# Performance work log

Measured on AMD Instinct MI355X. Metric: run time of the kernel, lower is better.

## Reference

```python
import jax, jax.numpy as jnp
import numpy as np

K = 3; STRIDE = 1; PAD = 1; DIL = 1; DG = 1


def _conv(x, w, b):
    y = jax.lax.conv_general_dilated(
        x, w, (STRIDE, STRIDE), [(PAD, PAD), (PAD, PAD)],
        dimension_numbers=("NCHW", "OIHW", "NCHW"))
    return y + b[None, :, None, None]


def _dcnv2(x, offset, mask, w, b):
    # x: [B,C,H,W]; offset: [B,2*DG*K*K,Ho,Wo]; mask: [B,DG*K*K,Ho,Wo] (post-sigmoid)
    B, C, H, W = x.shape
    Ho, Wo = offset.shape[2], offset.shape[3]
    KK = K * K
    Cdg = C // DG
    off = offset.reshape(B, DG, KK, 2, Ho, Wo)
    off_y, off_x = off[:, :, :, 0], off[:, :, :, 1]          # [B,DG,KK,Ho,Wo]
    m = mask.reshape(B, DG, KK, Ho, Wo)
    ky = (jnp.arange(KK) // K) * DIL
    kx = (jnp.arange(KK) % K) * DIL
    base_y = jnp.arange(Ho) * STRIDE - PAD
    base_x = jnp.arange(Wo) * STRIDE - PAD
    py = (base_y[None, :, None] + ky[:, None, None]).astype(x.dtype)  # [KK,Ho,1]
    px = (base_x[None, None, :] + kx[:, None, None]).astype(x.dtype)  # [KK,1,Wo]
    sy = py[None, None] + off_y                               # [B,DG,KK,Ho,Wo]
    sx = px[None, None] + off_x
    y0 = jnp.floor(sy); x0 = jnp.floor(sx)
    wy = sy - y0; wx = sx - x0
    feat = x.reshape(B, DG, Cdg, H * W)

    def corner(iy, ix):
        valid = (iy >= 0) & (iy <= H - 1) & (ix >= 0) & (ix <= W - 1)
        iyc = jnp.clip(iy, 0, H - 1).astype(jnp.int32)
        ixc = jnp.clip(ix, 0, W - 1).astype(jnp.int32)
        idx = (iyc * W + ixc).reshape(B, DG, KK * Ho * Wo)
        g = jax.vmap(jax.vmap(lambda f, i: f[:, i]))(feat, idx)  # [B,DG,Cdg,KK*Ho*Wo]
        g = g.reshape(B, DG, Cdg, KK, Ho, Wo)
        return g * valid[:, :, None].astype(x.dtype)

    one = jnp.asarray(1.0, x.dtype)
    v = (corner(y0, x0) * ((one - wy) * (one - wx))[:, :, None]
         + corner(y0, x0 + 1) * ((one - wy) * wx)[:, :, None]
         + corner(y0 + 1, x0) * (wy * (one - wx))[:, :, None]
         + corner(y0 + 1, x0 + 1) * (wy * wx)[:, :, None])
    v = v * m[:, :, None]                                     # modulation
    wg = w.reshape(w.shape[0], DG, Cdg, KK)                    # [Cout,DG,Cdg,KK]
    out = jnp.einsum("bgckhw,ogck->bohw", v, wg) + b[None, :, None, None]
    return out


def setup_inputs() -> dict:
    key = jax.random.key(0)
    k1, k2, k3 = jax.random.split(key, 3)
    B, C, H, W, Cout = 8, 256, 64, 64, 256
    x = jax.random.normal(k1, (B, C, H, W), jnp.float32)
    w_off = jax.random.normal(k2, (DG * 3 * K * K, C, K, K), jnp.float32) * 0.01
    b_off = jnp.zeros((DG * 3 * K * K,), jnp.float32)
    w_dcn = jax.random.normal(k3, (Cout, C, K, K), jnp.float32) * 0.02
    b_dcn = jnp.zeros((Cout,), jnp.float32)
    return {"x": x, "w_off": w_off, "b_off": b_off, "w_dcn": w_dcn, "b_dcn": b_dcn}


def reference(x, w_off, b_off, w_dcn, b_dcn):
    om = _conv(x, w_off, b_off)                # [B,3*DG*K*K,Ho,Wo]
    o1, o2, mask = jnp.split(om, 3, axis=1)
    offset = jnp.concatenate([o1, o2], axis=1)
    mask = jax.nn.sigmoid(mask)
    return _dcnv2(x, offset, mask, w_dcn, b_dcn)
```

## Files before the change

### kernel.cpp

```cpp
#include <hip/hip_runtime.h>
#include <math.h>

#define BB 8
#define CIN 256
#define HW 4096
#define BHW 32768
#define COUT 256
#define KTOT 2304
#define WS_N (BB*9*HW)

#define WOFF2_OFF (4*WS_N)
#define ACC_OFF   (WOFF2_OFF + 64512)
#define ATOMIC_NEED ((size_t)(ACC_OFF + 27*BHW) * 4)
#define XT_OFF    (ACC_OFF + 27*BHW)
#define NEED3     ((size_t)(XT_OFF + (BB*HW*CIN)/2) * 4)
#define WO16_OFF  (XT_OFF + (BB*HW*CIN)/2)
#define NEED4     ((size_t)(WO16_OFF + 36864) * 4)

#define PQ 520
#define NK2 36

typedef _Float16 hf;
typedef __attribute__((ext_vector_type(8))) _Float16 hfx8;
typedef __attribute__((ext_vector_type(4))) float f32x4;

__global__ __launch_bounds__(256) void prep_kernel(
    const float* __restrict__ x, const float* __restrict__ w_dcn,
    const float* __restrict__ w_off,
    hf* __restrict__ xt, hf* __restrict__ w16, hf* __restrict__ wo16)
{
  __shared__ float t[64][65];
  const int bx = blockIdx.x;
  const int tid = threadIdx.x;

  if (bx < 2048) {
    const int b  = bx >> 8;
    const int cb = (bx & 255) >> 6;
    const int pb = bx & 63;
    const int hi = tid >> 6, lo = tid & 63;
#pragma unroll
    for (int r = 0; r < 16; ++r) {
      int ci = r * 4 + hi;
      t[ci][lo] = x[((size_t)(b * 256 + cb * 64 + ci)) * HW + pb * 64 + lo];
    }
    __syncthreads();
#pragma unroll
    for (int r = 0; r < 16; ++r) {
      int p = r * 4 + hi;
      xt[((size_t)(b * HW + pb * 64 + p)) * 256 + cb * 64 + lo] = (hf)t[lo][p];
    }
  } else if (bx < 2048 + 256) {
    const int co = bx - 2048;
    const int c  = tid;
    const int cblk = c >> 5, cin = c & 31, q = cin >> 3, j = cin & 7;
#pragma unroll
    for (int kk = 0; kk < 9; ++kk)
      w16[(size_t)(cblk * 9 + kk) * 8192 + (q * 256 + co) * 8 + j] =
        (hf)w_dcn[(size_t)co * KTOT + c * 9 + kk];
  } else {
    const int ks = bx - 2304;
    const int cblk = ks / 9, kk = ks - cblk * 9;
    for (int idx = tid; idx < 1024; idx += 256) {
      int lk = idx >> 8, row = (idx >> 3) & 31, j = idx & 7;
      int c = cblk * 32 + lk * 8 + j;
      float v = (row < 27) ? w_off[(size_t)row * KTOT + c * 9 + kk] : 0.f;
      wo16[(size_t)ks * 1024 + idx] = (hf)v;
    }
  }
}

__global__ __launch_bounds__(256, 2) void dcn_fused_kernel(
    const hf* __restrict__ xt, const hf* __restrict__ w16,
    const hf* __restrict__ wo16, const float* __restrict__ b_off,
    const float* __restrict__ b_dcn, float* __restrict__ out)
{
  __shared__ hf B_lds[2][8 * PQ];
  __shared__ int2   pidx[576];
  __shared__ float4 pwts[576];

  const int tid  = threadIdx.x;
  const int b    = blockIdx.x & 7;
  const int pos0 = (blockIdx.x >> 3) * 64;

  const int lane = tid & 63, wid = tid >> 6;
  const int lm = lane & 15, lk = lane >> 4;
  const int gp = tid >> 2;
  const int gh = tid & 3;
  const int gpos = pos0 + gp;
  const int gho = gpos >> 6, gwo = gpos & 63;

  const hf* bt = xt + (size_t)b * HW * 256;
  const hfx8 zv = {};

  {
    f32x4 oacc[2];
    oacc[0] = (f32x4){0.f, 0.f, 0.f, 0.f};
    oacc[1] = (f32x4){0.f, 0.f, 0.f, 0.f};
    const hf* wga = wo16 + ((lk * 32 + lm) << 3);

    hfx8 gA, gB;
    bool vA, vB;

#define OG(S, T, CB)                                                     \
    {                                                                    \
      int ky = (T) / 3, kx = (T) - 3 * (ky);                             \
      int yy = gho + ky - 1, xx = gwo + kx - 1;                          \
      v##S = ((unsigned)yy < 64u) && ((unsigned)xx < 64u);               \
      int row = gpos + (ky - 1) * 64 + (kx - 1);                         \
      row = min(max(row, 0), HW - 1);                                    \
      g##S = *(const hfx8*)(bt + ((size_t)row << 8) + (CB) + gh * 8);    \
    }

    OG(A, 0, 0); OG(B, 1, 0);
    *(hfx8*)&B_lds[0][gh * PQ + gp * 8]       = vA ? gA : zv;
    *(hfx8*)&B_lds[0][(4 + gh) * PQ + gp * 8] = vB ? gB : zv;
    OG(A, 2, 0); OG(B, 3, 0);
    asm volatile("s_waitcnt lgkmcnt(0)" ::: "memory");
    __builtin_amdgcn_sched_barrier(0);
    __builtin_amdgcn_s_barrier();

#pragma unroll 2
    for (int i = 0; i < NK2 - 1; ++i) {
      const int ri = i & 1, wi = ri ^ 1;
      const hf* wg0 = wga + (size_t)(2 * i) * 1024;
      hfx8 af00 = *(const hfx8*)(wg0);
      hfx8 af01 = *(const hfx8*)(wg0 + 128);
      hfx8 af10 = *(const hfx8*)(wg0 + 1024);
      hfx8 af11 = *(const hfx8*)(wg0 + 1024 + 128);

      hfx8 bf0 = *(const hfx8*)&B_lds[ri][lk * PQ + (wid * 16 + lm) * 8];
      hfx8 bf1 = *(const hfx8*)&B_lds[ri][(4 + lk) * PQ + (wid * 16 + lm) * 8];

      *(hfx8*)&B_lds[wi][gh * PQ + gp * 8]       = vA ? gA : zv;
      *(hfx8*)&B_lds[wi][(4 + gh) * PQ + gp * 8] = vB ? gB : zv;

      {
        int ks0 = 2 * i + 4; if (ks0 > 70) ks0 = 70;
        int dA = ks0 / 9; int tA = ks0 - dA * 9; int cbA = dA * 32;
        int ks1 = ks0 + 1;
        int dB = ks1 / 9; int tB = ks1 - dB * 9; int cbB = dB * 32;
        OG(A, tA, cbA); OG(B, tB, cbB);
      }

      oacc[0] = __builtin_amdgcn_mfma_f32_16x16x32_f16(af00, bf0, oacc[0], 0, 0, 0);
      oacc[1] = __builtin_amdgcn_mfma_f32_16x16x32_f16(af01, bf0, oacc[1], 0, 0, 0);
      oacc[0] = __builtin_amdgcn_mfma_f32_16x16x32_f16(af10, bf1, oacc[0], 0, 0, 0);
      oacc[1] = __builtin_amdgcn_mfma_f32_16x16x32_f16(af11, bf1, oacc[1], 0, 0, 0);

      asm volatile("s_waitcnt lgkmcnt(0)" ::: "memory");
      __builtin_amdgcn_sched_barrier(0);
      __builtin_amdgcn_s_barrier();
    }

    {
      const hf* wg0 = wga + (size_t)70 * 1024;
      hfx8 af00 = *(const hfx8*)(wg0);
      hfx8 af01 = *(const hfx8*)(wg0 + 128);
      hfx8 af10 = *(const hfx8*)(wg0 + 1024);
      hfx8 af11 = *(const hfx8*)(wg0 + 1024 + 128);
      hfx8 bf0 = *(const hfx8*)&B_lds[1][lk * PQ + (wid * 16 + lm) * 8];
      hfx8 bf1 = *(const hfx8*)&B_lds[1][(4 + lk) * PQ + (wid * 16 + lm) * 8];
      oacc[0] = __builtin_amdgcn_mfma_f32_16x16x32_f16(af00, bf0, oacc[0], 0, 0, 0);
      oacc[1] = __builtin_amdgcn_mfma_f32_16x16x32_f16(af01, bf0, oacc[1], 0, 0, 0);
      oacc[0] = __builtin_amdgcn_mfma_f32_16x16x32_f16(af10, bf1, oacc[0], 0, 0, 0);
      oacc[1] = __builtin_amdgcn_mfma_f32_16x16x32_f16(af11, bf1, oacc[1], 0, 0, 0);
    }
#undef OG

    float* stage = (float*)&B_lds[0][0];
    __syncthreads();
#pragma unroll
    for (int fr = 0; fr < 2; ++fr)
#pragma unroll
      for (int r = 0; r < 4; ++r)
        stage[(fr * 16 + lk * 4 + r) * 66 + wid * 16 + lm] = oacc[fr][r];
    __syncthreads();
    for (int t = tid; t < 576; t += 256) {
      int kk = t >> 6, p = t & 63;
      int pos = pos0 + p;
      int ho = pos >> 6, wo = pos & 63;
      float sy = stage[(2 * kk) * 66 + p]     + b_off[2 * kk]     + (float)(ho - 1 + kk / 3);
      float sx = stage[(2 * kk + 1) * 66 + p] + b_off[2 * kk + 1] + (float)(wo - 1 + kk % 3);
      float mv = stage[(18 + kk) * 66 + p]    + b_off[18 + kk];
      float m  = 1.f / (1.f + expf(-mv));
      float y0f = floorf(sy), x0f = floorf(sx);
      int y0 = (int)y0f, x0 = (int)x0f;
      float wy = sy - y0f, wx = sx - x0f;
      int ix0 = min(max(x0, 0), 63), ix1 = min(max(x0 + 1, 0), 63);
      int bx  = min(max(x0, 0), 62);
      float vx0 = (x0 >= 0  && x0 <= 63) ? 1.f : 0.f;
      float vx1 = (x0 >= -1 && x0 <= 62) ? 1.f : 0.f;
      float wx0 = (1.f - wx) * vx0, wx1 = wx * vx1;
      float a0 = (ix0 == bx     ? wx0 : 0.f) + (ix1 == bx     ? wx1 : 0.f);
      float a1 = (ix0 == bx + 1 ? wx0 : 0.f) + (ix1 == bx + 1 ? wx1 : 0.f);
      int rb0 = min(max(y0, 0), 63), rb1 = min(max(y0 + 1, 0), 63);
      float vy0 = (y0 >= 0  && y0 <= 63) ? 1.f : 0.f;
      float vy1 = (y0 >= -1 && y0 <= 62) ? 1.f : 0.f;
      float wy0m = (1.f - wy) * vy0 * m, wy1m = wy * vy1 * m;
      pidx[t] = make_int2(rb0 * 64 + bx, rb1 * 64 + bx);
      pwts[t] = make_float4(a0 * wy0m, a1 * wy0m, a0 * wy1m, a1 * wy1m);
    }
    __syncthreads();
  }

  const int chq = tid & 3;

  f32x4 acc[4][4];
#pragma unroll
  for (int a = 0; a < 4; ++a)
#pragma unroll
    for (int c = 0; c < 4; ++c)
      acc[a][c] = (f32x4){0.f, 0.f, 0.f, 0.f};

  const hf* wga = w16 + ((lk * 256 + wid * 64 + lm) << 3);
  const int wA = chq * PQ + gp * 8;
  const int wB = (4 + chq) * PQ + gp * 8;

  hf hwA0, hwA1, hwA2, hwA3, hwB0, hwB1, hwB2, hwB3;
  hfx8 cA00, cA01, cA10, cA11, cB00, cB01, cB10, cB11;

#define GATH(S, T, CB)                                                   \
  {                                                                      \
    int pb = (T) * 64 + gp;                                              \
    int2 pi = pidx[pb]; float4 pw = pwts[pb];                            \
    hw##S##0 = (hf)pw.x; hw##S##1 = (hf)pw.y;                            \
    hw##S##2 = (hf)pw.z; hw##S##3 = (hf)pw.w;                            \
    const hf* p0 = bt + ((size_t)pi.x << 8) + (CB) + (chq << 3);         \
    const hf* p1 = bt + ((size_t)pi.y << 8) + (CB) + (chq << 3);         \
    c##S##00 = *(const hfx8*)p0; c##S##01 = *(const hfx8*)(p0 + 256);    \
    c##S##10 = *(const hfx8*)p1; c##S##11 = *(const hfx8*)(p1 + 256);    \
  }

#define COMB(S, DST)                                                     \
  {                                                                      \
    hfx8 vv = c##S##00 * hw##S##0;                                       \
    vv += c##S##01 * hw##S##1;                                           \
    vv += c##S##10 * hw##S##2;                                           \
    vv += c##S##11 * hw##S##3;                                           \
    *(hfx8*)(DST) = vv;                                                  \
  }

  GATH(A, 0, 0); GATH(B, 1, 0);
  COMB(A, &B_lds[0][wA]);
  COMB(B, &B_lds[0][wB]);
  GATH(A, 2, 0); GATH(B, 3, 0);
  asm volatile("s_waitcnt lgkmcnt(0)" ::: "memory");
  __builtin_amdgcn_sched_barrier(0);
  __builtin_amdgcn_s_barrier();

#pragma unroll 2
  for (int i = 0; i < NK2 - 1; ++i) {
    const int ri = i & 1, wi = ri ^ 1;

    const hf* wg0 = wga + (size_t)(2 * i) * 8192;
    hfx8 af0[4], af1[4];
#pragma unroll
    for (int fr = 0; fr < 4; ++fr) af0[fr] = *(const hfx8*)(wg0 + fr * 128);

    hfx8 bf0[4], bf1[4];
#pragma unroll
    for (int pf = 0; pf < 4; ++pf)
      bf0[pf] = *(const hfx8*)&B_lds[ri][lk * PQ + (pf * 16 + lm) * 8];
#pragma unroll
    for (int fr = 0; fr < 4; ++fr) af1[fr] = *(const hfx8*)(wg0 + 8192 + fr * 128);
#pragma unroll
    for (int pf = 0; pf < 4; ++pf)
      bf1[pf] = *(const hfx8*)&B_lds[ri][(4 + lk) * PQ + (pf * 16 + lm) * 8];

    COMB(A, &B_lds[wi][wA]);
    COMB(B, &B_lds[wi][wB]);

    {
      int ks0 = 2 * i + 4; if (ks0 > 70) ks0 = 70;
      int dA = ks0 / 9; int tA = ks0 - dA * 9; int cbA = dA * 32;
      int ks1 = ks0 + 1;
      int dB = ks1 / 9; int tB = ks1 - dB * 9; int cbB = dB * 32;
      GATH(A, tA, cbA); GATH(B, tB, cbB);
    }

#pragma unroll
    for (int fr = 0; fr < 4; ++fr)
#pragma unroll
      for (int pf = 0; pf < 4; ++pf)
        acc[fr][pf] = __builtin_amdgcn_mfma_f32_16x16x32_f16(af0[fr], bf0[pf], acc[fr][pf], 0, 0, 0);
#pragma unroll
    for (int fr = 0; fr < 4; ++fr)
#pragma unroll
      for (int pf = 0; pf < 4; ++pf)
        acc[fr][pf] = __builtin_amdgcn_mfma_f32_16x16x32_f16(af1[fr], bf1[pf], acc[fr][pf], 0, 0, 0);

    asm volatile("s_waitcnt lgkmcnt(0)" ::: "memory");
    __builtin_amdgcn_sched_barrier(0);
    __builtin_amdgcn_s_barrier();
  }

  {
    const hf* wg0 = wga + (size_t)70 * 8192;
    hfx8 af0[4], af1[4];
#pragma unroll
    for (int fr = 0; fr < 4; ++fr) af0[fr] = *(const hfx8*)(wg0 + fr * 128);
#pragma unroll
    for (int fr = 0; fr < 4; ++fr) af1[fr] = *(const hfx8*)(wg0 + 8192 + fr * 128);
    hfx8 bf0[4], bf1[4];
#pragma unroll
    for (int pf = 0; pf < 4; ++pf) {
      bf0[pf] = *(const hfx8*)&B_lds[1][lk * PQ + (pf * 16 + lm) * 8];
      bf1[pf] = *(const hfx8*)&B_lds[1][(4 + lk) * PQ + (pf * 16 + lm) * 8];
    }
#pragma unroll
    for (int fr = 0; fr < 4; ++fr)
#pragma unroll
      for (int pf = 0; pf < 4; ++pf)
        acc[fr][pf] = __builtin_amdgcn_mfma_f32_16x16x32_f16(af0[fr], bf0[pf], acc[fr][pf], 0, 0, 0);
#pragma unroll
    for (int fr = 0; fr < 4; ++fr)
#pragma unroll
      for (int pf = 0; pf < 4; ++pf)
        acc[fr][pf] = __builtin_amdgcn_mfma_f32_16x16x32_f16(af1[fr], bf1[pf], acc[fr][pf], 0, 0, 0);
  }
#undef GATH
#undef COMB

#pragma unroll
  for (int fr = 0; fr < 4; ++fr) {
#pragma unroll
    for (int r = 0; r < 4; ++r) {
      int co = wid * 64 + fr * 16 + lk * 4 + r;
      float bias = b_dcn[co];
      float* orow = out + ((size_t)b * COUT + co) * HW + pos0;
#pragma unroll
      for (int pf = 0; pf < 4; ++pf)
        orow[pf * 16 + lm] = acc[fr][pf][r] + bias;
    }
  }
}

extern "C" void kernel_launch(void* const* d_in, const int* in_sizes, int n_in,
                              void* d_out, int out_size, void* d_ws, size_t ws_size,
                              hipStream_t stream) {
  const float* x     = (const float*)d_in[0];
  const float* w_off = (const float*)d_in[1];
  const float* b_off = (const float*)d_in[2];
  const float* w_dcn = (const float*)d_in[3];
  const float* b_dcn = (const float*)d_in[4];
  float* out = (float*)d_out;
  float* ws  = (float*)d_ws;
  hf* w16  = (hf*)(ws + 3 * WS_N);

  hf* xt;
  hf* wo16;
  if (ws_size >= NEED4) {
    xt   = (hf*)(ws + XT_OFF);
    wo16 = (hf*)(ws + WO16_OFF);
  } else {
    xt   = (hf*)ws;
    wo16 = (hf*)(ws + (BB * HW * CIN) / 2);
  }

  prep_kernel<<<2376, 256, 0, stream>>>(x, w_dcn, w_off, xt, w16, wo16);
  dcn_fused_kernel<<<BB * (HW / 64), 256, 0, stream>>>(xt, w16, wo16, b_off, b_dcn, out);
}
```

Measured before the change: 82.60 us.

## Merge two 64-position tiles into one 512-thread block

Each block now runs 512 threads as two independent 256-thread halves, each handling its own 64-position tile with separate LDS buffers, and the grid is halved. The likely aim is better sharing of the weight fragments through cache between the two halves and fewer, larger blocks. Barriers now synchronise both halves together, which can add stalls. The bigger per-block LDS footprint may also limit occupancy under the (512,2) launch bounds. The stage stride also changes from 66 to 65.

```diff
diff --git a/kernel.cpp b/kernel.cpp
--- a/kernel.cpp
+++ b/kernel.cpp
@@ -9,9 +9,7 @@
 #define KTOT 2304
 #define WS_N (BB*9*HW)
 
-#define WOFF2_OFF (4*WS_N)
-#define ACC_OFF   (WOFF2_OFF + 64512)
-#define ATOMIC_NEED ((size_t)(ACC_OFF + 27*BHW) * 4)
+#define ACC_OFF   (4*WS_N + 64512)
 #define XT_OFF    (ACC_OFF + 27*BHW)
 #define NEED3     ((size_t)(XT_OFF + (BB*HW*CIN)/2) * 4)
 #define WO16_OFF  (XT_OFF + (BB*HW*CIN)/2)
@@ -69,24 +67,29 @@
   }
 }
 
-__global__ __launch_bounds__(256, 2) void dcn_fused_kernel(
+__global__ __launch_bounds__(512, 2) void dcn_fused2_kernel(
     const hf* __restrict__ xt, const hf* __restrict__ w16,
     const hf* __restrict__ wo16, const float* __restrict__ b_off,
     const float* __restrict__ b_dcn, float* __restrict__ out)
 {
-  __shared__ hf B_lds[2][8 * PQ];
-  __shared__ int2   pidx[576];
-  __shared__ float4 pwts[576];
+  __shared__ hf B_lds[2][2][8 * PQ];
+  __shared__ int2   pidx[2][576];
+  __shared__ float4 pwts[2][576];
 
   const int tid  = threadIdx.x;
   const int b    = blockIdx.x & 7;
-  const int pos0 = (blockIdx.x >> 3) * 64;
-
-  const int lane = tid & 63, wid = tid >> 6;
+  const int pos0 = (blockIdx.x >> 3) * 128;
+
+  const int hh   = tid >> 8;
+  const int t8   = tid & 255;
+  const int pos0h = pos0 + hh * 64;
+
+  const int lane = tid & 63;
+  const int wid4 = (tid >> 6) & 3;
   const int lm = lane & 15, lk = lane >> 4;
-  const int gp = tid >> 2;
-  const int gh = tid & 3;
-  const int gpos = pos0 + gp;
+  const int gp = t8 >> 2;
+  const int gh = t8 & 3;
+  const int gpos = pos0h + gp;
   const int gho = gpos >> 6, gwo = gpos & 63;
 
   const hf* bt = xt + (size_t)b * HW * 256;
@@ -112,8 +115,8 @@
     }
 
     OG(A, 0, 0); OG(B, 1, 0);
-    *(hfx8*)&B_lds[0][gh * PQ + gp * 8]       = vA ? gA : zv;
-    *(hfx8*)&B_lds[0][(4 + gh) * PQ + gp * 8] = vB ? gB : zv;
+    *(hfx8*)&B_lds[hh][0][gh * PQ + gp * 8]       = vA ? gA : zv;
+    *(hfx8*)&B_lds[hh][0][(4 + gh) * PQ + gp * 8] = vB ? gB : zv;
     OG(A, 2, 0); OG(B, 3, 0);
     asm volatile("s_waitcnt lgkmcnt(0)" ::: "memory");
     __builtin_amdgcn_sched_barrier(0);
@@ -128,11 +131,11 @@
       hfx8 af10 = *(const hfx8*)(wg0 + 1024);
       hfx8 af11 = *(const hfx8*)(wg0 + 1024 + 128);
 
-      hfx8 bf0 = *(const hfx8*)&B_lds[ri][lk * PQ + (wid * 16 + lm) * 8];
-      hfx8 bf1 = *(const hfx8*)&B_lds[ri][(4 + lk) * PQ + (wid * 16 + lm) * 8];
-
-      *(hfx8*)&B_lds[wi][gh * PQ + gp * 8]       = vA ? gA : zv;
-      *(hfx8*)&B_lds[wi][(4 + gh) * PQ + gp * 8] = vB ? gB : zv;
+      hfx8 bf0 = *(const hfx8*)&B_lds[hh][ri][lk * PQ + (wid4 * 16 + lm) * 8];
+      hfx8 bf1 = *(const hfx8*)&B_lds[hh][ri][(4 + lk) * PQ + (wid4 * 16 + lm) * 8];
+
+      *(hfx8*)&B_lds[hh][wi][gh * PQ + gp * 8]       = vA ? gA : zv;
+      *(hfx8*)&B_lds[hh][wi][(4 + gh) * PQ + gp * 8] = vB ? gB : zv;
 
       {
         int ks0 = 2 * i + 4; if (ks0 > 70) ks0 = 70;
@@ -158,8 +161,8 @@
       hfx8 af01 = *(const hfx8*)(wg0 + 128);
       hfx8 af10 = *(const hfx8*)(wg0 + 1024);
       hfx8 af11 = *(const hfx8*)(wg0 + 1024 + 128);
-      hfx8 bf0 = *(const hfx8*)&B_lds[1][lk * PQ + (wid * 16 + lm) * 8];
-      hfx8 bf1 = *(const hfx8*)&B_lds[1][(4 + lk) * PQ + (wid * 16 + lm) * 8];
+      hfx8 bf0 = *(const hfx8*)&B_lds[hh][1][lk * PQ + (wid4 * 16 + lm) * 8];
+      hfx8 bf1 = *(const hfx8*)&B_lds[hh][1][(4 + lk) * PQ + (wid4 * 16 + lm) * 8];
       oacc[0] = __builtin_amdgcn_mfma_f32_16x16x32_f16(af00, bf0, oacc[0], 0, 0, 0);
       oacc[1] = __builtin_amdgcn_mfma_f32_16x16x32_f16(af01, bf0, oacc[1], 0, 0, 0);
       oacc[0] = __builtin_amdgcn_mfma_f32_16x16x32_f16(af10, bf1, oacc[0], 0, 0, 0);
@@ -167,21 +170,21 @@
     }
 #undef OG
 
-    float* stage = (float*)&B_lds[0][0];
+    float* stage = (float*)&B_lds[hh][0][0];
     __syncthreads();
 #pragma unroll
     for (int fr = 0; fr < 2; ++fr)
 #pragma unroll
       for (int r = 0; r < 4; ++r)
-        stage[(fr * 16 + lk * 4 + r) * 66 + wid * 16 + lm] = oacc[fr][r];
+        stage[(fr * 16 + lk * 4 + r) * 65 + wid4 * 16 + lm] = oacc[fr][r];
     __syncthreads();
-    for (int t = tid; t < 576; t += 256) {
+    for (int t = t8; t < 576; t += 256) {
       int kk = t >> 6, p = t & 63;
-      int pos = pos0 + p;
+      int pos = pos0h + p;
       int ho = pos >> 6, wo = pos & 63;
-      float sy = stage[(2 * kk) * 66 + p]     + b_off[2 * kk]     + (float)(ho - 1 + kk / 3);
-      float sx = stage[(2 * kk + 1) * 66 + p] + b_off[2 * kk + 1] + (float)(wo - 1 + kk % 3);
-      float mv = stage[(18 + kk) * 66 + p]    + b_off[18 + kk];
+      float sy = stage[(2 * kk) * 65 + p]     + b_off[2 * kk]     + (float)(ho - 1 + kk / 3);
+      float sx = stage[(2 * kk + 1) * 65 + p] + b_off[2 * kk + 1] + (float)(wo - 1 + kk % 3);
+      float mv = stage[(18 + kk) * 65 + p]    + b_off[18 + kk];
       float m  = 1.f / (1.f + expf(-mv));
       float y0f = floorf(sy), x0f = floorf(sx);
       int y0 = (int)y0f, x0 = (int)x0f;
@@ -197,13 +200,13 @@
       float vy0 = (y0 >= 0  && y0 <= 63) ? 1.f : 0.f;
       float vy1 = (y0 >= -1 && y0 <= 62) ? 1.f : 0.f;
       float wy0m = (1.f - wy) * vy0 * m, wy1m = wy * vy1 * m;
-      pidx[t] = make_int2(rb0 * 64 + bx, rb1 * 64 + bx);
-      pwts[t] = make_float4(a0 * wy0m, a1 * wy0m, a0 * wy1m, a1 * wy1m);
+      pidx[hh][t] = make_int2(rb0 * 64 + bx, rb1 * 64 + bx);
+      pwts[hh][t] = make_float4(a0 * wy0m, a1 * wy0m, a0 * wy1m, a1 * wy1m);
     }
     __syncthreads();
   }
 
-  const int chq = tid & 3;
+  const int chq = t8 & 3;
 
   f32x4 acc[4][4];
 #pragma unroll
@@ -212,7 +215,7 @@
     for (int c = 0; c < 4; ++c)
       acc[a][c] = (f32x4){0.f, 0.f, 0.f, 0.f};
 
-  const hf* wga = w16 + ((lk * 256 + wid * 64 + lm) << 3);
+  const hf* wga = w16 + ((lk * 256 + wid4 * 64 + lm) << 3);
   const int wA = chq * PQ + gp * 8;
   const int wB = (4 + chq) * PQ + gp * 8;
 
@@ -222,7 +225,7 @@
 #define GATH(S, T, CB)                                                   \
   {                                                                      \
     int pb = (T) * 64 + gp;                                              \
-    int2 pi = pidx[pb]; float4 pw = pwts[pb];                            \
+    int2 pi = pidx[hh][pb]; float4 pw = pwts[hh][pb];                    \
     hw##S##0 = (hf)pw.x; hw##S##1 = (hf)pw.y;                            \
     hw##S##2 = (hf)pw.z; hw##S##3 = (hf)pw.w;                            \
     const hf* p0 = bt + ((size_t)pi.x << 8) + (CB) + (chq << 3);         \
@@ -241,8 +244,8 @@
   }
 
   GATH(A, 0, 0); GATH(B, 1, 0);
-  COMB(A, &B_lds[0][wA]);
-  COMB(B, &B_lds[0][wB]);
+  COMB(A, &B_lds[hh][0][wA]);
+  COMB(B, &B_lds[hh][0][wB]);
   GATH(A, 2, 0); GATH(B, 3, 0);
   asm volatile("s_waitcnt lgkmcnt(0)" ::: "memory");
   __builtin_amdgcn_sched_barrier(0);
@@ -260,15 +263,15 @@
     hfx8 bf0[4], bf1[4];
 #pragma unroll
     for (int pf = 0; pf < 4; ++pf)
-      bf0[pf] = *(const hfx8*)&B_lds[ri][lk * PQ + (pf * 16 + lm) * 8];
+      bf0[pf] = *(const hfx8*)&B_lds[hh][ri][lk * PQ + (pf * 16 + lm) * 8];
 #pragma unroll
     for (int fr = 0; fr < 4; ++fr) af1[fr] = *(const hfx8*)(wg0 + 8192 + fr * 128);
 #pragma unroll
     for (int pf = 0; pf < 4; ++pf)
-      bf1[pf] = *(const hfx8*)&B_lds[ri][(4 + lk) * PQ + (pf * 16 + lm) * 8];
-
-    COMB(A, &B_lds[wi][wA]);
-    COMB(B, &B_lds[wi][wB]);
+      bf1[pf] = *(const hfx8*)&B_lds[hh][ri][(4 + lk) * PQ + (pf * 16 + lm) * 8];
+
+    COMB(A, &B_lds[hh][wi][wA]);
+    COMB(B, &B_lds[hh][wi][wB]);
 
     {
       int ks0 = 2 * i + 4; if (ks0 > 70) ks0 = 70;
@@ -304,8 +307,8 @@
     hfx8 bf0[4], bf1[4];
 #pragma unroll
     for (int pf = 0; pf < 4; ++pf) {
-      bf0[pf] = *(const hfx8*)&B_lds[1][lk * PQ + (pf * 16 + lm) * 8];
-      bf1[pf] = *(const hfx8*)&B_lds[1][(4 + lk) * PQ + (pf * 16 + lm) * 8];
+      bf0[pf] = *(const hfx8*)&B_lds[hh][1][lk * PQ + (pf * 16 + lm) * 8];
+      bf1[pf] = *(const hfx8*)&B_lds[hh][1][(4 + lk) * PQ + (pf * 16 + lm) * 8];
     }
 #pragma unroll
     for (int fr = 0; fr < 4; ++fr)
@@ -325,9 +328,9 @@
   for (int fr = 0; fr < 4; ++fr) {
 #pragma unroll
     for (int r = 0; r < 4; ++r) {
-      int co = wid * 64 + fr * 16 + lk * 4 + r;
+      int co = wid4 * 64 + fr * 16 + lk * 4 + r;
       float bias = b_dcn[co];
-      float* orow = out + ((size_t)b * COUT + co) * HW + pos0;
+      float* orow = out + ((size_t)b * COUT + co) * HW + pos0h;
 #pragma unroll
       for (int pf = 0; pf < 4; ++pf)
         orow[pf * 16 + lm] = acc[fr][pf][r] + bias;
@@ -358,5 +361,5 @@
   }
 
   prep_kernel<<<2376, 256, 0, stream>>>(x, w_dcn, w_off, xt, w16, wo16);
-  dcn_fused_kernel<<<BB * (HW / 64), 256, 0, stream>>>(xt, w16, wo16, b_off, b_dcn, out);
+  dcn_fused2_kernel<<<BB * (HW / 128), 512, 0, stream>>>(xt, w16, wo16, b_off, b_dcn, out);
 }
```

Result: slower. 91.89 us (+11.2%).
